# Kernel optimization log

Measured on AMD Instinct MI355X. Metric: run time of the kernel, lower is better.

The kernel has to match this reference:

```python
import jax, jax.numpy as jnp
import numpy as np

N_NODES = 10000
N_EDGES = 160000
N_GRAPHS = 20
IN_F, HID, OUT_F, HEADS = 50, 256, 121, 4
NEG_SLOPE = 0.2
GN_EPS = 1e-5
SM_EPS = 1e-16


def _with_self_loops(edge_index, n):
    loop = jnp.arange(n, dtype=edge_index.dtype)
    src = jnp.concatenate([edge_index[0], loop])
    dst = jnp.concatenate([edge_index[1], loop])
    return src, dst


def gat_conv(x, W, att_src, att_dst, bias, src, dst, heads, out_c):
    # PyG GATConv: linear -> per-node attention halves -> edge leaky_relu
    # -> softmax over incoming edges of each dst -> weighted scatter-sum.
    n = x.shape[0]
    h = (x @ W).reshape(n, heads, out_c)                # [N,H,C]
    a_s = (h * att_src).sum(-1)                          # [N,H]
    a_d = (h * att_dst).sum(-1)                          # [N,H]
    e = a_s[src] + a_d[dst]                              # [E,H]
    e = jnp.where(e > 0, e, NEG_SLOPE * e)
    e_max = jax.ops.segment_max(e, dst, num_segments=n)  # self-loops cover all dst
    ex = jnp.exp(e - e_max[dst])
    den = jax.ops.segment_sum(ex, dst, num_segments=n)
    alpha = ex / (den[dst] + SM_EPS)                     # [E,H]
    out = jax.ops.segment_sum(h[src] * alpha[..., None], dst, num_segments=n)
    return out.reshape(n, heads * out_c) + bias


def graph_norm(x, batch, weight, bias, mean_scale, n_graphs):
    cnt = jax.ops.segment_sum(jnp.ones((x.shape[0],), x.dtype), batch,
                              num_segments=n_graphs)[:, None]    # [G,1]
    mean = jax.ops.segment_sum(x, batch, num_segments=n_graphs) / cnt
    ctr = x - mean[batch] * mean_scale
    var = jax.ops.segment_sum(ctr * ctr, batch, num_segments=n_graphs) / cnt
    inv = jax.lax.rsqrt(var + GN_EPS)
    return weight * ctr * inv[batch] + bias


def setup_inputs() -> dict:
    key = jax.random.key(0)
    ks = jax.random.split(key, 24)
    d = {}
    d['x'] = jax.random.normal(ks[0], (N_NODES, IN_F), jnp.float32)
    d['edge_index'] = jax.random.randint(ks[1], (2, N_EDGES), 0, N_NODES, jnp.int64 if jax.config.jax_enable_x64 else jnp.int32)
    d['batch'] = jnp.sort(jax.random.randint(ks[2], (N_NODES,), 0, N_GRAPHS))
    def glorot(k, shape):
        fan = shape[0] + shape[-1]
        return jax.random.normal(k, shape, jnp.float32) * np.sqrt(2.0 / fan)
    dims = [(IN_F, HEADS, HID), (HEADS * HID, HEADS, HID), (HEADS * HID, HEADS, HID), (HEADS * HID, 1, OUT_F)]
    i = 3
    for li, (fin, h, c) in enumerate(dims, 1):
        d[f'W{li}'] = glorot(ks[i], (fin, h * c)); i += 1
        d[f'as{li}'] = glorot(ks[i], (h, c)); i += 1
        d[f'ad{li}'] = glorot(ks[i], (h, c)); i += 1
        d[f'b{li}'] = jnp.zeros((h * c,), jnp.float32)
    for li in (1, 2, 3):
        w = HEADS * HID
        d[f'gw{li}'] = jnp.ones((w,), jnp.float32)
        d[f'gb{li}'] = jnp.zeros((w,), jnp.float32)
        d[f'ga{li}'] = jnp.ones((w,), jnp.float32)
    return d


def reference(x, edge_index, batch,
              W1, as1, ad1, b1, W2, as2, ad2, b2, W3, as3, ad3, b3, W4, as4, ad4, b4,
              gw1, gb1, ga1, gw2, gb2, ga2, gw3, gb3, ga3):
    src, dst = _with_self_loops(edge_index, N_NODES)
    h = gat_conv(x, W1, as1, ad1, b1, src, dst, HEADS, HID)
    h = jax.nn.elu(graph_norm(h, batch, gw1, gb1, ga1, N_GRAPHS))
    h = gat_conv(h, W2, as2, ad2, b2, src, dst, HEADS, HID)
    h = jax.nn.elu(graph_norm(h, batch, gw2, gb2, ga2, N_GRAPHS))
    h = gat_conv(h, W3, as3, ad3, b3, src, dst, HEADS, HID)
    h = jax.nn.elu(graph_norm(h, batch, gw3, gb3, ga3, N_GRAPHS))
    return gat_conv(h, W4, as4, ad4, b4, src, dst, 1, OUT_F)
```

## Files before the change

### kernel.cpp

```cpp
#include <hip/hip_runtime.h>
#include <math.h>

#define NN 10000
#define NE 160000
#define E2 (NE + NN)
#define NG 20
#define MPAD 10112

typedef __attribute__((ext_vector_type(8))) short short8;
typedef __attribute__((ext_vector_type(4))) float f32x4;

__device__ inline unsigned short f2bf(float f){
  unsigned u = __float_as_uint(f);
  unsigned r = u + 0x7FFFu + ((u >> 16) & 1u);
  return (unsigned short)(r >> 16);
}
__device__ inline float bf2f(unsigned short h){ return __uint_as_float(((unsigned)h) << 16); }

__device__ inline void gload_lds16(const void* g, void* l){
  __builtin_amdgcn_global_load_lds((const __attribute__((address_space(1))) void*)g,
                                   (__attribute__((address_space(3))) void*)l, 16, 0, 0);
}

__global__ void k_gptr(const int* __restrict__ batch, int* __restrict__ gptr){
  int g = threadIdx.x;
  if (g > NG) return;
  int lo = 0, hi = NN;
  while (lo < hi){ int mid = (lo+hi)>>1; if (batch[mid] < g) lo = mid+1; else hi = mid; }
  gptr[g] = lo;
}

__global__ void k_count(const int* __restrict__ ei, int* __restrict__ cnt){
  int e = blockIdx.x*256 + threadIdx.x;
  if (e >= E2) return;
  int d = (e < NE) ? ei[NE + e] : (e - NE);
  atomicAdd(&cnt[d], 1);
}

__global__ void k_scan(const int* __restrict__ cnt, int* __restrict__ ptr){
  __shared__ int tpre[256];
  __shared__ int tsum[256];
  int tid = threadIdx.x;
  const int per = (NN + 255)/256;
  int base = tid*per;
  int s = 0;
  for (int i=0;i<per;i++){ int idx=base+i; if (idx<NN) s += cnt[idx]; }
  tsum[tid] = s;
  __syncthreads();
  if (tid == 0){
    int run = 0;
    for (int i=0;i<256;i++){ tpre[i]=run; run += tsum[i]; }
    ptr[NN] = run;
  }
  __syncthreads();
  int run = tpre[tid];
  for (int i=0;i<per;i++){ int idx=base+i; if (idx<NN){ ptr[idx]=run; run += cnt[idx]; } }
}

__global__ void k_copy(const int* __restrict__ src, int* __restrict__ dst){
  int i = blockIdx.x*256 + threadIdx.x;
  if (i < NN) dst[i] = src[i];
}

__global__ void k_scatter(const int* __restrict__ ei, int* __restrict__ fill, int* __restrict__ csrc){
  int e = blockIdx.x*256 + threadIdx.x;
  if (e >= E2) return;
  int s, d;
  if (e < NE){ s = ei[e]; d = ei[NE + e]; } else { s = d = e - NE; }
  int pos = atomicAdd(&fill[d], 1);
  csrc[pos] = s;
}

__global__ void k_xconv(const float* __restrict__ x, unsigned short* __restrict__ xbf){
  int i = blockIdx.x*256 + threadIdx.x;
  if (i >= MPAD*64) return;
  int r = i >> 6, c = i & 63;
  float v = (r < NN && c < 50) ? x[r*50 + c] : 0.f;
  xbf[i] = f2bf(v);
}

__global__ void k_wconv(const float* __restrict__ W, unsigned short* __restrict__ Wt,
                        int K, int N, int Kpad, int Npad){
  int i = blockIdx.x*256 + threadIdx.x;
  if (i >= Npad*Kpad) return;
  int nn = i / Kpad, kk = i - nn*Kpad;
  float v = (nn < N && kk < K) ? W[(size_t)kk*N + nn] : 0.f;
  Wt[i] = f2bf(v);
}

template<int TBM, int TBN>
__global__ __launch_bounds__(256) void k_mfma_gemm(
    const unsigned short* __restrict__ A,
    const unsigned short* __restrict__ Bt,
    unsigned short* __restrict__ Cbf,
    int M, int K, int FS, int ncb)
{
  constexpr int MFR = TBM/32;
  constexpr int NFR = TBN/32;
  constexpr int ABYTES = TBM*64;
  constexpr int BBYTES = TBN*64;
  __shared__ unsigned short sA[2*TBM*32];
  __shared__ unsigned short sB[2*TBN*32];
  const int tid = threadIdx.x;
  const int wave = tid >> 6;
  const int lane = tid & 63;
  const int nwg = gridDim.x;
  const int q = nwg >> 3, rmod = nwg & 7;
  const int xcd = blockIdx.x & 7, idx = blockIdx.x >> 3;
  const int wg = (xcd < rmod) ? (xcd*(q+1) + idx) : (rmod*(q+1) + (xcd - rmod)*q + idx);
  const int rowt = wg / ncb;
  const int colt = wg - rowt*ncb;
  const int row0 = rowt * TBM;
  const int col0 = colt * TBN;
  const int wr = (wave >> 1) * (TBM/2);
  const int wc = (wave & 1) * (TBN/2);
  f32x4 acc[MFR][NFR];
  #pragma unroll
  for (int i=0;i<MFR;i++)
    #pragma unroll
    for (int j=0;j<NFR;j++){ acc[i][j][0]=0.f; acc[i][j][1]=0.f; acc[i][j][2]=0.f; acc[i][j][3]=0.f; }

  const int arow = tid >> 2;
  const int achn = (tid & 3) ^ ((arow >> 1) & 3);
  const unsigned short* aSrc = A + (size_t)(row0 + arow)*K + achn*8;
  const unsigned short* bSrc = Bt + (size_t)(col0 + arow)*K + achn*8;
  char* ldsA = (char*)sA + wave*1024;
  char* ldsB = (char*)sB + wave*1024;

  auto STAGE = [&](int k0, int buf){
    #pragma unroll
    for (int h=0; h<TBM/64; h++) gload_lds16(aSrc + (size_t)h*64*K + k0, ldsA + buf*ABYTES + h*4096);
    #pragma unroll
    for (int h=0; h<TBN/64; h++) gload_lds16(bSrc + (size_t)h*64*K + k0, ldsB + buf*BBYTES + h*4096);
  };

  const int NT = K >> 5;
  const int kch = lane >> 4;
  const int rlo = lane & 15;

  STAGE(0, 0);
  if (NT > 1) STAGE(32, 1);
  if constexpr (TBM+TBN == 256) asm volatile("s_waitcnt vmcnt(4)" ::: "memory");
  else                          asm volatile("s_waitcnt vmcnt(2)" ::: "memory");
  __builtin_amdgcn_sched_barrier(0);
  __builtin_amdgcn_s_barrier();

  int cur = 0;
  for (int t = 0; t < NT; ++t){
    const unsigned short* bA = sA + cur*(TBM*32);
    const unsigned short* bB = sB + cur*(TBN*32);
    short8 af[MFR], bfr[NFR];
    #pragma unroll
    for (int m=0;m<MFR;m++){
      int r = wr + m*16 + rlo;
      af[m] = *(const short8*)(bA + r*32 + ((kch ^ ((r>>1)&3))<<3));
    }
    #pragma unroll
    for (int n=0;n<NFR;n++){
      int r = wc + n*16 + rlo;
      bfr[n] = *(const short8*)(bB + r*32 + ((kch ^ ((r>>1)&3))<<3));
    }
    asm volatile("s_waitcnt lgkmcnt(0)" ::: "memory");
    __builtin_amdgcn_sched_barrier(0);
    __builtin_amdgcn_s_barrier();
    if (t+2 < NT) STAGE((t+2) << 5, cur);
    #pragma unroll
    for (int m=0;m<MFR;m++)
      #pragma unroll
      for (int n=0;n<NFR;n++)
        acc[m][n] = __builtin_amdgcn_mfma_f32_16x16x32_bf16(af[m], bfr[n], acc[m][n], 0, 0, 0);
    if (t+1 < NT){
      if (t+2 < NT){
        if constexpr (TBM+TBN == 256) asm volatile("s_waitcnt vmcnt(4)" ::: "memory");
        else                          asm volatile("s_waitcnt vmcnt(2)" ::: "memory");
      } else {
        asm volatile("s_waitcnt vmcnt(0)" ::: "memory");
      }
      __builtin_amdgcn_sched_barrier(0);
      __builtin_amdgcn_s_barrier();
    }
    cur ^= 1;
  }
  const int cr = (lane >> 4) * 4;
  const int cc = lane & 15;
  #pragma unroll
  for (int m=0;m<MFR;m++){
    #pragma unroll
    for (int n=0;n<NFR;n++){
      int col = col0 + wc + n*16 + cc;
      #pragma unroll
      for (int r=0;r<4;r++){
        int row = row0 + wr + m*16 + cr + r;
        if (row < M) Cbf[(size_t)row*FS + col] = f2bf(acc[m][n][r]);
      }
    }
  }
}

__global__ void k_attprep(const unsigned short* __restrict__ h, const float* __restrict__ atts,
                          const float* __restrict__ attd,
                          float* __restrict__ a_s, float* __restrict__ a_d, int H, int C, int FS){
  int node = blockIdx.x, head = blockIdx.y;
  int lane = threadIdx.x;
  const unsigned short* hp = h + (size_t)node*FS + head*C;
  const float* sp = atts + head*C;
  const float* dp = attd + head*C;
  float ss = 0.f, sd = 0.f;
  for (int c = lane; c < C; c += 64){ float v = bf2f(hp[c]); ss += v*sp[c]; sd += v*dp[c]; }
  #pragma unroll
  for (int o = 32; o; o >>= 1){ ss += __shfl_down(ss, o); sd += __shfl_down(sd, o); }
  if (lane == 0){ a_s[node*H + head] = ss; a_d[node*H + head] = sd; }
}

__global__ void k_alpha(const float* __restrict__ a_s, const float* __restrict__ a_d,
                        const int* __restrict__ ptr, const int* __restrict__ csrc,
                        float* __restrict__ alphaT, int H, int LH){
  int node = blockIdx.x;
  int lane = threadIdx.x;
  int beg = ptr[node], deg = ptr[node+1] - beg;
  int items = deg << LH;
  int hh = lane & (H-1);
  float ad = a_d[node*H + hh];
  float mx = -INFINITY;
  for (int i = lane; i < items; i += 64){
    int e = i >> LH;
    int s = csrc[beg + e];
    float ev = a_s[s*H + hh] + ad;
    ev = ev > 0.f ? ev : 0.2f*ev;
    mx = fmaxf(mx, ev);
  }
  for (int o = H; o < 64; o <<= 1) mx = fmaxf(mx, __shfl_xor(mx, o));
  float den = 0.f;
  for (int i = lane; i < items; i += 64){
    int e = i >> LH;
    int s = csrc[beg + e];
    float ev = a_s[s*H + hh] + ad;
    ev = ev > 0.f ? ev : 0.2f*ev;
    den += __expf(ev - mx);
  }
  for (int o = H; o < 64; o <<= 1) den += __shfl_xor(den, o);
  float inv = 1.f / (den + 1e-16f);
  for (int i = lane; i < items; i += 64){
    int e = i >> LH;
    int s = csrc[beg + e];
    float ev = a_s[s*H + hh] + ad;
    ev = ev > 0.f ? ev : 0.2f*ev;
    alphaT[(size_t)hh*E2 + beg + e] = __expf(ev - mx) * inv;
  }
}

template<int L>
__global__ __launch_bounds__(256) void k_gather2(
    const unsigned short* __restrict__ h, int FS,
    const float* __restrict__ alphaT,
    const int* __restrict__ ptr, const int* __restrict__ csrc,
    const float* __restrict__ bias, float* __restrict__ out,
    int F, int C, int outF)
{
  constexpr int NGRP = 256 / L;
  constexpr int CS = L * 8;
  const int node = blockIdx.x;
  const int head = blockIdx.y;
  const int colbase = head * C;
  const int beg = ptr[node], deg = ptr[node+1] - beg;
  __shared__ int ssrc[256];
  __shared__ float sal[256];
  __shared__ float red[NGRP * CS];
  const int tid = threadIdx.x;
  const int grp = tid / L, li = tid % L;
  const int c0 = colbase + li*8;
  const float* aT = alphaT + (size_t)head*E2 + beg;
  float acc[8] = {0.f,0.f,0.f,0.f,0.f,0.f,0.f,0.f};
  for (int b0 = 0; b0 < deg; b0 += 256){
    int bn = min(256, deg - b0);
    if (tid < bn){ ssrc[tid] = csrc[beg + b0 + tid]; sal[tid] = aT[b0 + tid]; }
    __syncthreads();
    for (int e = grp; e < bn; e += NGRP){
      int s = ssrc[e];
      float al = sal[e];
      short8 v = *(const short8*)(h + (size_t)s*FS + c0);
      #pragma unroll
      for (int j=0;j<8;j++) acc[j] += bf2f((unsigned short)v[j]) * al;
    }
    __syncthreads();
  }
  #pragma unroll
  for (int j=0;j<8;j++) red[grp*CS + li*8 + j] = acc[j];
  __syncthreads();
  for (int c = tid; c < CS; c += 256){
    float s = 0.f;
    #pragma unroll
    for (int g=0; g<NGRP; g++) s += red[g*CS + c];
    int oc = colbase + c;
    if (oc < F) out[(size_t)node*outF + oc] = s + bias[oc];
  }
}

#define NSPLIT 16
__global__ void k_gnstats(const float* __restrict__ x, const int* __restrict__ gptr,
                          float* __restrict__ gsum, float* __restrict__ gsq, int F){
  int g = blockIdx.x, cc = blockIdx.y, sp = blockIdx.z;
  int c = cc*256 + threadIdx.x;
  if (c >= F) return;
  int beg = gptr[g], end = gptr[g+1];
  int n = end - beg;
  int per = (n + NSPLIT - 1) / NSPLIT;
  int nb = beg + sp*per, ne = min(end, nb + per);
  if (ne <= nb) return;
  float s = 0.f, q = 0.f;
  for (int i = nb; i < ne; i++){ float v = x[(size_t)i*F + c]; s += v; q += v*v; }
  atomicAdd(&gsum[g*F + c], s);
  atomicAdd(&gsq[g*F + c], q);
}

__global__ void k_coef(const float* __restrict__ gsum, const float* __restrict__ gsq, const int* __restrict__ gptr,
                       const float* __restrict__ w, const float* __restrict__ b, const float* __restrict__ ms,
                       float* __restrict__ cA, float* __restrict__ cB, int F){
  int i = blockIdx.x*256 + threadIdx.x;
  if (i >= NG*F) return;
  int g = i / F, c = i - g*F;
  float cntf = (float)(gptr[g+1] - gptr[g]);
  float m = gsum[i] / cntf;
  float s = ms[c];
  float ex2 = gsq[i] / cntf;
  float var = ex2 - 2.f*s*m*m + s*s*m*m;
  float inv = rsqrtf(var + 1e-5f);
  float wa = w[c]*inv;
  cA[i] = wa;
  cB[i] = b[c] - wa*m*s;
}

__global__ void k_applyelu(const float* __restrict__ x, const int* __restrict__ batch,
                           const float* __restrict__ cA, const float* __restrict__ cB,
                           unsigned short* __restrict__ obf, int F){
  size_t i = (size_t)blockIdx.x*256 + threadIdx.x;
  if (i >= (size_t)NN*F) return;
  int node = (int)(i / F);
  int c = (int)(i - (size_t)node*F);
  int g = batch[node];
  float y = cA[g*F + c]*x[i] + cB[g*F + c];
  y = y > 0.f ? y : expm1f(y);
  obf[i] = f2bf(y);
}

extern "C" void kernel_launch(void* const* d_in, const int* in_sizes, int n_in,
                              void* d_out, int out_size, void* d_ws, size_t ws_size,
                              hipStream_t stream){
  (void)in_sizes; (void)n_in; (void)out_size; (void)ws_size;
  const float* x     = (const float*)d_in[0];
  const int*   ei    = (const int*)d_in[1];
  const int*   batch = (const int*)d_in[2];
  const float* W[4]  = {(const float*)d_in[3],  (const float*)d_in[7],  (const float*)d_in[11], (const float*)d_in[15]};
  const float* AS[4] = {(const float*)d_in[4],  (const float*)d_in[8],  (const float*)d_in[12], (const float*)d_in[16]};
  const float* AD[4] = {(const float*)d_in[5],  (const float*)d_in[9],  (const float*)d_in[13], (const float*)d_in[17]};
  const float* BI[4] = {(const float*)d_in[6],  (const float*)d_in[10], (const float*)d_in[14], (const float*)d_in[18]};
  const float* GW[3] = {(const float*)d_in[19], (const float*)d_in[22], (const float*)d_in[25]};
  const float* GB[3] = {(const float*)d_in[20], (const float*)d_in[23], (const float*)d_in[26]};
  const float* GA[3] = {(const float*)d_in[21], (const float*)d_in[24], (const float*)d_in[27]};

  float* ws   = (float*)d_ws;
  float* bufB = ws;
  float* a_s  = bufB + (size_t)NN*1024;
  float* a_d  = a_s + (size_t)NN*4;
  float* gsum = a_d + (size_t)NN*4;
  float* gsq  = gsum + (size_t)NG*1024;
  float* cA   = gsq  + (size_t)NG*1024;
  float* cB   = cA   + (size_t)NG*1024;
  float* alphaT = cB + (size_t)NG*1024;
  int* ptr  = (int*)(alphaT + (size_t)4*E2);
  int* fill = ptr + (NN + 8);
  int* csrc = fill + (NN + 8);
  int* gptr = csrc + E2;
  unsigned short* xbf = (unsigned short*)(gptr + 24);
  unsigned short* abf = xbf + (size_t)MPAD*64;
  unsigned short* hbf = abf + (size_t)MPAD*1024;
  unsigned short* Wt  = hbf + (size_t)NN*1024;

  hipMemsetAsync(fill, 0, sizeof(int)*(NN+1), stream);
  k_gptr<<<1, 32, 0, stream>>>(batch, gptr);
  k_count<<<(E2+255)/256, 256, 0, stream>>>(ei, fill);
  k_scan<<<1, 256, 0, stream>>>(fill, ptr);
  k_copy<<<(NN+255)/256, 256, 0, stream>>>(ptr, fill);
  k_scatter<<<(E2+255)/256, 256, 0, stream>>>(ei, fill, csrc);
  k_xconv<<<(MPAD*64+255)/256, 256, 0, stream>>>(x, xbf);

  const int Kp[4]  = {64, 1024, 1024, 1024};
  const int Kr[4]  = {50, 1024, 1024, 1024};
  const int Np[4]  = {1024, 1024, 1024, 128};
  for (int li = 0; li < 4; ++li){
    int H = (li == 3) ? 1 : 4;
    int LH = (li == 3) ? 0 : 2;
    int C = (li == 3) ? 121 : 256;
    int F = H*C;
    int FS = Np[li];
    const unsigned short* Ain = (li == 0) ? xbf : abf;
    k_wconv<<<(Np[li]*Kp[li]+255)/256, 256, 0, stream>>>(W[li], Wt, Kr[li], F, Kp[li], Np[li]);
    if (li < 3){
      int ncb = Np[li]/128;
      int nwg = (MPAD/128) * ncb;
      k_mfma_gemm<128,128><<<nwg, 256, 0, stream>>>(Ain, Wt, hbf, NN, Kp[li], FS, ncb);
    } else {
      int ncb = Np[li]/64;
      int nwg = (MPAD/64) * ncb;
      k_mfma_gemm<64,64><<<nwg, 256, 0, stream>>>(Ain, Wt, hbf, NN, Kp[li], FS, ncb);
    }
    k_attprep<<<dim3(NN, H), 64, 0, stream>>>(hbf, AS[li], AD[li], a_s, a_d, H, C, FS);
    k_alpha<<<NN, 64, 0, stream>>>(a_s, a_d, ptr, csrc, alphaT, H, LH);
    float* gout = (li == 3) ? (float*)d_out : bufB;
    if (li < 3)
      k_gather2<32><<<dim3(NN, 4), 256, 0, stream>>>(hbf, FS, alphaT, ptr, csrc, BI[li], gout, F, C, F);
    else
      k_gather2<16><<<dim3(NN, 1), 256, 0, stream>>>(hbf, FS, alphaT, ptr, csrc, BI[li], gout, F, C, F);
    if (li < 3){
      hipMemsetAsync(gsum, 0, sizeof(float)*2*NG*1024, stream);
      k_gnstats<<<dim3(NG, (F+255)/256, NSPLIT), 256, 0, stream>>>(bufB, gptr, gsum, gsq, F);
      k_coef<<<(NG*F + 255)/256, 256, 0, stream>>>(gsum, gsq, gptr, GW[li], GB[li], GA[li], cA, cB, F);
      size_t tot = (size_t)NN*F;
      k_applyelu<<<(unsigned)((tot + 255)/256), 256, 0, stream>>>(bufB, batch, cA, cB, abf, F);
    }
  }
}
```

Measured before the change: 550.7 us.

## Use 64x128 GEMM tiles, vectorize attprep, add per-node all-heads gather kernel

The first three layers now use a 64x128 GEMM tile, which doubles the workgroup count to fill more compute units, and the vmcnt waits are generalized to the new load count. k_attprep uses vectorized 4-wide loads when C is 256. A new k_gather3 replaces the per-head gather with one block per node covering all four heads. Each thread loads 8 bf16 values and two edge groups are reduced through shared memory. This cuts repeated csrc and pointer reads and the launch count, at the cost of more shared memory and a lower per-tile reuse in the GEMM.

```diff
diff --git a/kernel.cpp b/kernel.cpp
--- a/kernel.cpp
+++ b/kernel.cpp
@@ -8,6 +8,7 @@
 #define MPAD 10112
 
 typedef __attribute__((ext_vector_type(8))) short short8;
+typedef __attribute__((ext_vector_type(4))) short short4v;
 typedef __attribute__((ext_vector_type(4))) float f32x4;
 
 __device__ inline unsigned short f2bf(float f){
@@ -99,6 +100,7 @@
   constexpr int NFR = TBN/32;
   constexpr int ABYTES = TBM*64;
   constexpr int BBYTES = TBN*64;
+  constexpr int LPS = TBM/64 + TBN/64;
   __shared__ unsigned short sA[2*TBM*32];
   __shared__ unsigned short sB[2*TBN*32];
   const int tid = threadIdx.x;
@@ -140,8 +142,9 @@
 
   STAGE(0, 0);
   if (NT > 1) STAGE(32, 1);
-  if constexpr (TBM+TBN == 256) asm volatile("s_waitcnt vmcnt(4)" ::: "memory");
-  else                          asm volatile("s_waitcnt vmcnt(2)" ::: "memory");
+  if constexpr (LPS==4)      asm volatile("s_waitcnt vmcnt(4)" ::: "memory");
+  else if constexpr (LPS==3) asm volatile("s_waitcnt vmcnt(3)" ::: "memory");
+  else                       asm volatile("s_waitcnt vmcnt(2)" ::: "memory");
   __builtin_amdgcn_sched_barrier(0);
   __builtin_amdgcn_s_barrier();
 
@@ -171,8 +174,9 @@
         acc[m][n] = __builtin_amdgcn_mfma_f32_16x16x32_bf16(af[m], bfr[n], acc[m][n], 0, 0, 0);
     if (t+1 < NT){
       if (t+2 < NT){
-        if constexpr (TBM+TBN == 256) asm volatile("s_waitcnt vmcnt(4)" ::: "memory");
-        else                          asm volatile("s_waitcnt vmcnt(2)" ::: "memory");
+        if constexpr (LPS==4)      asm volatile("s_waitcnt vmcnt(4)" ::: "memory");
+        else if constexpr (LPS==3) asm volatile("s_waitcnt vmcnt(3)" ::: "memory");
+        else                       asm volatile("s_waitcnt vmcnt(2)" ::: "memory");
       } else {
         asm volatile("s_waitcnt vmcnt(0)" ::: "memory");
       }
@@ -202,11 +206,20 @@
                           float* __restrict__ a_s, float* __restrict__ a_d, int H, int C, int FS){
   int node = blockIdx.x, head = blockIdx.y;
   int lane = threadIdx.x;
-  const unsigned short* hp = h + (size_t)node*FS + head*C;
-  const float* sp = atts + head*C;
-  const float* dp = attd + head*C;
   float ss = 0.f, sd = 0.f;
-  for (int c = lane; c < C; c += 64){ float v = bf2f(hp[c]); ss += v*sp[c]; sd += v*dp[c]; }
+  if (C == 256){
+    const unsigned short* hp = h + (size_t)node*FS + head*256 + lane*4;
+    short4v v = *(const short4v*)hp;
+    f32x4 sp = *(const f32x4*)(atts + head*256 + lane*4);
+    f32x4 dp = *(const f32x4*)(attd + head*256 + lane*4);
+    #pragma unroll
+    for (int j=0;j<4;j++){ float f = bf2f((unsigned short)v[j]); ss += f*sp[j]; sd += f*dp[j]; }
+  } else {
+    const unsigned short* hp = h + (size_t)node*FS + head*C;
+    const float* sp = atts + head*C;
+    const float* dp = attd + head*C;
+    for (int c = lane; c < C; c += 64){ float v = bf2f(hp[c]); ss += v*sp[c]; sd += v*dp[c]; }
+  }
   #pragma unroll
   for (int o = 32; o; o >>= 1){ ss += __shfl_down(ss, o); sd += __shfl_down(sd, o); }
   if (lane == 0){ a_s[node*H + head] = ss; a_d[node*H + head] = sd; }
@@ -246,6 +259,61 @@
     float ev = a_s[s*H + hh] + ad;
     ev = ev > 0.f ? ev : 0.2f*ev;
     alphaT[(size_t)hh*E2 + beg + e] = __expf(ev - mx) * inv;
+  }
+}
+
+__global__ __launch_bounds__(256) void k_gather3(
+    const unsigned short* __restrict__ h,
+    const float* __restrict__ alphaT,
+    const int* __restrict__ ptr, const int* __restrict__ csrc,
+    const float* __restrict__ bias, float* __restrict__ out)
+{
+  const int node = blockIdx.x;
+  const int beg = ptr[node], deg = ptr[node+1] - beg;
+  const int tid = threadIdx.x;
+  const int li = tid & 127;
+  const int grp = tid >> 7;
+  const int head = li >> 5;
+  const int c0 = li * 8;
+  __shared__ int ssrc[128];
+  __shared__ float sal[4][128];
+  __shared__ float red[2][1024];
+  float acc[8] = {0.f,0.f,0.f,0.f,0.f,0.f,0.f,0.f};
+  for (int b0 = 0; b0 < deg; b0 += 128){
+    int bn = min(128, deg - b0);
+    if (tid < bn){
+      ssrc[tid] = csrc[beg + b0 + tid];
+      #pragma unroll
+      for (int hh=0; hh<4; hh++) sal[hh][tid] = alphaT[(size_t)hh*E2 + beg + b0 + tid];
+    }
+    __syncthreads();
+    int e = grp;
+    for (; e + 2 < bn; e += 4){
+      int s0 = ssrc[e], s1 = ssrc[e+2];
+      float a0 = sal[head][e], a1 = sal[head][e+2];
+      short8 v0 = *(const short8*)(h + (size_t)s0*1024 + c0);
+      short8 v1 = *(const short8*)(h + (size_t)s1*1024 + c0);
+      #pragma unroll
+      for (int j=0;j<8;j++) acc[j] += bf2f((unsigned short)v0[j])*a0;
+      #pragma unroll
+      for (int j=0;j<8;j++) acc[j] += bf2f((unsigned short)v1[j])*a1;
+    }
+    if (e < bn){
+      int s0 = ssrc[e];
+      float a0 = sal[head][e];
+      short8 v0 = *(const short8*)(h + (size_t)s0*1024 + c0);
+      #pragma unroll
+      for (int j=0;j<8;j++) acc[j] += bf2f((unsigned short)v0[j])*a0;
+    }
+    __syncthreads();
+  }
+  #pragma unroll
+  for (int j=0;j<8;j++) red[grp][c0+j] = acc[j];
+  __syncthreads();
+  #pragma unroll
+  for (int k=0;k<4;k++){
+    int c = tid + k*256;
+    out[(size_t)node*1024 + c] = red[0][c] + red[1][c] + bias[c];
   }
 }
 
@@ -397,8 +465,8 @@
     k_wconv<<<(Np[li]*Kp[li]+255)/256, 256, 0, stream>>>(W[li], Wt, Kr[li], F, Kp[li], Np[li]);
     if (li < 3){
       int ncb = Np[li]/128;
-      int nwg = (MPAD/128) * ncb;
-      k_mfma_gemm<128,128><<<nwg, 256, 0, stream>>>(Ain, Wt, hbf, NN, Kp[li], FS, ncb);
+      int nwg = (MPAD/64) * ncb;
+      k_mfma_gemm<64,128><<<nwg, 256, 0, stream>>>(Ain, Wt, hbf, NN, Kp[li], FS, ncb);
     } else {
       int ncb = Np[li]/64;
       int nwg = (MPAD/64) * ncb;
@@ -408,7 +476,7 @@
     k_alpha<<<NN, 64, 0, stream>>>(a_s, a_d, ptr, csrc, alphaT, H, LH);
     float* gout = (li == 3) ? (float*)d_out : bufB;
     if (li < 3)
-      k_gather2<32><<<dim3(NN, 4), 256, 0, stream>>>(hbf, FS, alphaT, ptr, csrc, BI[li], gout, F, C, F);
+      k_gather3<<<NN, 256, 0, stream>>>(hbf, alphaT, ptr, csrc, BI[li], gout);
     else
       k_gather2<16><<<dim3(NN, 1), 256, 0, stream>>>(hbf, FS, alphaT, ptr, csrc, BI[li], gout, F, C, F);
     if (li < 3){
```

After: 550.7 us. No clear change (+0.0%).
